# Optimization experiments

Hardware: AMD Instinct MI355X
Metric: run time of the kernel (lower is better)

## Reference

```python
import jax, jax.numpy as jnp
import numpy as np

N_NODES, N_EDGES, D_FEAT, D_HID, K_CHEB = 30000, 480000, 256, 256, 2


def setup_inputs() -> dict:
    N, E, D, H, K = N_NODES, N_EDGES, D_FEAT, D_HID, K_CHEB
    key = jax.random.key(0)
    ks = jax.random.split(key, 24)
    sD = 1.0 / np.sqrt(D)
    sH = 1.0 / np.sqrt(H)
    inp = {
        "x": jax.random.normal(ks[0], (N, D), jnp.float32),
        "edge_index": jax.random.randint(ks[1], (2, E), 0, N),
        "edge_weight": jax.random.uniform(ks[2], (E,), jnp.float32),
        "h": jax.random.normal(ks[3], (N, H), jnp.float32),
        "c": jax.random.normal(ks[4], (N, H), jnp.float32),
        "src_neighbor_ids": jax.random.randint(ks[5], (E,), 0, N),
        "dst_neighbor_ids": jax.random.randint(ks[6], (E,), 0, N),
    }
    for j, nm in enumerate(["W_i", "W_f", "W_g", "W_o"]):
        inp[nm] = jax.random.normal(ks[7 + j], (D, H), jnp.float32) * sD
    for j, nm in enumerate(["Wc_i", "Wc_f", "Wc_g", "Wc_o"]):
        inp[nm] = jax.random.normal(ks[11 + j], (K, H, H), jnp.float32) * sH
    for nm in ["bc_i", "bc_f", "bc_g", "bc_o", "b_i", "b_f", "b_g", "b_o", "b_lin"]:
        inp[nm] = jnp.zeros((H,), jnp.float32)
    for j, nm in enumerate(["w_ci", "w_cf", "w_co"]):
        inp[nm] = jax.random.normal(ks[15 + j], (H,), jnp.float32) * 0.1
    inp["W_lin"] = jax.random.normal(ks[18], (H, H), jnp.float32) * sH
    return inp


def _cheb_conv(h, src, dst, norm, W, b):
    # ChebConv, K=2, sym norm, lambda_max=2: T0 = h, T1 = L_hat h = -D^-1/2 A D^-1/2 h
    out = h @ W[0]
    t1 = jax.ops.segment_sum(norm[:, None] * h[src], dst, num_segments=h.shape[0])
    return out + t1 @ W[1] + b


def reference(x, edge_index, edge_weight, h, c, src_neighbor_ids, dst_neighbor_ids,
              W_i, W_f, W_g, W_o, Wc_i, Wc_f, Wc_g, Wc_o,
              bc_i, bc_f, bc_g, bc_o, w_ci, w_cf, w_co,
              b_i, b_f, b_g, b_o, W_lin, b_lin):
    src, dst = edge_index[0], edge_index[1]
    n = x.shape[0]
    # neighbor-feature augmentation: gather both BEFORE any update, then scatter-add
    snf = x[src_neighbor_ids]
    dnf = x[dst_neighbor_ids]
    x = x.at[src].add(snf)
    x = x.at[dst].add(dnf)
    # symmetric Chebyshev normalization (lambda_max = 2 -> diagonal of L_hat is 0)
    deg = jax.ops.segment_sum(edge_weight, src, num_segments=n)
    dinv = jnp.where(deg > 0, jax.lax.rsqrt(jnp.maximum(deg, 1e-12)), 0.0)
    norm = -dinv[src] * edge_weight * dinv[dst]
    # GCLSTM gates
    i = jax.nn.sigmoid(x @ W_i + _cheb_conv(h, src, dst, norm, Wc_i, bc_i) + w_ci * c + b_i)
    f = jax.nn.sigmoid(x @ W_f + _cheb_conv(h, src, dst, norm, Wc_f, bc_f) + w_cf * c + b_f)
    g = jnp.tanh(x @ W_g + _cheb_conv(h, src, dst, norm, Wc_g, bc_g) + b_g)
    c_new = f * c + i * g
    o = jax.nn.sigmoid(x @ W_o + _cheb_conv(h, src, dst, norm, Wc_o, bc_o) + w_co * c_new + b_o)
    h0 = o * jnp.tanh(c_new)
    h_out = jax.nn.relu(h0) @ W_lin + b_lin
    return (h_out, h0, c_new)
```

## Files before the change

kernel.cpp:

```cpp
#include <hip/hip_runtime.h>
#include <math.h>

#define NN 30000
#define NE 480000
#define DH 256
#define NH (NN * DH)
#define MPAD 30080
#define CAP 64

typedef _Float16 f16x2 __attribute__((ext_vector_type(2)));
typedef _Float16 f16x4 __attribute__((ext_vector_type(4)));
typedef _Float16 f16x8 __attribute__((ext_vector_type(8)));
typedef float f32x4 __attribute__((ext_vector_type(4)));

static __device__ __forceinline__ float sigmoidf_(float x) {
    return 1.0f / (1.0f + __expf(-x));
}
static __device__ __forceinline__ float tanhf_(float x) {
    return 1.0f - 2.0f / (1.0f + __expf(2.0f * x));
}

static __device__ __forceinline__ void gload16(const _Float16* g, _Float16* l) {
    __builtin_amdgcn_global_load_lds(
        (const __attribute__((address_space(1))) void*)g,
        (__attribute__((address_space(3))) void*)l, 16, 0, 0);
}


__global__ void deg_kernel(const int* __restrict__ src, const float* __restrict__ ew,
                           float* __restrict__ deg) {
    int e = blockIdx.x * blockDim.x + threadIdx.x;
    if (e < NE) atomicAdd(&deg[src[e]], ew[e]);
}


__global__ void mega1(const int* __restrict__ src, const int* __restrict__ dst,
                      const int* __restrict__ snf, const int* __restrict__ dnf,
                      const float* __restrict__ ew, const float* __restrict__ deg,
                      int* __restrict__ cntS, int* __restrict__ cntD,
                      int* __restrict__ slotS, int2* __restrict__ slotD,
                      const float* __restrict__ x, _Float16* __restrict__ x16,
                      const float* __restrict__ h, _Float16* __restrict__ h16,
                      const float* __restrict__ W_i, const float* __restrict__ W_f,
                      const float* __restrict__ W_g, const float* __restrict__ W_o,
                      const float* __restrict__ Wc_i, const float* __restrict__ Wc_f,
                      const float* __restrict__ Wc_g, const float* __restrict__ Wc_o,
                      const float* __restrict__ W_lin,
                      const float* __restrict__ bc_i, const float* __restrict__ bc_f,
                      const float* __restrict__ bc_g, const float* __restrict__ bc_o,
                      const float* __restrict__ b_i, const float* __restrict__ b_f,
                      const float* __restrict__ b_g, const float* __restrict__ b_o,
                      const float* __restrict__ w_ci, const float* __restrict__ w_cf,
                      const float* __restrict__ w_co,
                      _Float16* __restrict__ WcatT, _Float16* __restrict__ WlinT,
                      float4* __restrict__ bias4, float4* __restrict__ wc4) {
    int b = blockIdx.x;
    if (b < 1875) {
        int e = b * 256 + threadIdx.x;
        int s = src[e], d = dst[e];
        int pS = atomicAdd(&cntS[s], 1);
        if (pS < CAP) slotS[s * CAP + pS] = snf[e];
        float ds_ = deg[s], dd_ = deg[d];
        float is_ = (ds_ > 0.0f) ? rsqrtf(fmaxf(ds_, 1e-12f)) : 0.0f;
        float id_ = (dd_ > 0.0f) ? rsqrtf(fmaxf(dd_, 1e-12f)) : 0.0f;
        float nrm = -is_ * ew[e] * id_;
        int pD = atomicAdd(&cntD[d], 1);
        if (pD < CAP) slotD[d * CAP + pD] = make_int2(s | (dnf[e] << 15), __float_as_int(nrm));
        return;
    }
    b -= 1875;
    if (b < 7500) {
        int i = b * 256 + threadIdx.x;
        const int n8 = NN * 32;
        const float* in; _Float16* out; int idx;
        if (i < n8) { in = x; out = x16; idx = i; }
        else { in = h; out = h16; idx = i - n8; }
        const float4 p = *reinterpret_cast<const float4*>(&in[(size_t)idx * 8]);
        const float4 q = *reinterpret_cast<const float4*>(&in[(size_t)idx * 8 + 4]);
        f16x8 v;
        v[0] = (_Float16)p.x; v[1] = (_Float16)p.y; v[2] = (_Float16)p.z; v[3] = (_Float16)p.w;
        v[4] = (_Float16)q.x; v[5] = (_Float16)q.y; v[6] = (_Float16)q.z; v[7] = (_Float16)q.w;
        *reinterpret_cast<f16x8*>(&out[(size_t)idx * 8]) = v;
        return;
    }
    b -= 7500;
    int idx = b * 256 + threadIdx.x;
    if (idx < 768 * 1024) {
        int k = idx >> 10, n = idx & 1023;
        int seg = k >> 8, kk = k & 255, nn = n >> 2, gate = n & 3;
        const float* p;
        if (seg == 0) {
            p = (gate == 0) ? W_i : (gate == 1) ? W_f : (gate == 2) ? W_g : W_o;
        } else {
            const float* base = (gate == 0) ? Wc_i : (gate == 1) ? Wc_f : (gate == 2) ? Wc_g : Wc_o;
            p = base + (seg - 1) * 65536;
        }
        WcatT[(size_t)n * 768 + k] = (_Float16)p[kk * 256 + nn];
    } else if (idx < 768 * 1024 + 256 * 256) {
        int i2 = idx - 768 * 1024;
        int k = i2 >> 8, n = i2 & 255;
        WlinT[(size_t)n * 256 + k] = (_Float16)W_lin[k * 256 + n];
    } else {
        int f = idx - (768 * 1024 + 256 * 256);
        bias4[f] = make_float4(bc_i[f] + b_i[f], bc_f[f] + b_f[f],
                               bc_g[f] + b_g[f], bc_o[f] + b_o[f]);
        wc4[f] = make_float4(w_ci[f], w_cf[f], w_co[f], 0.f);
    }
}


__global__ __launch_bounds__(256) void fused_gather(const _Float16* __restrict__ x16,
                                                    const _Float16* __restrict__ h16,
                                                    const int* __restrict__ cntS,
                                                    const int* __restrict__ cntD,
                                                    const int4* __restrict__ slotS4,
                                                    const int4* __restrict__ slotD4,
                                                    _Float16* __restrict__ A16) {
    int wid = (blockIdx.x * blockDim.x + threadIdx.x) >> 6;
    int l = threadIdx.x & 63;
    if (wid >= MPAD) return;
    size_t rb = (size_t)wid * 768;
    if (wid >= NN) {
        f16x4 z = {};
        *reinterpret_cast<f16x4*>(&A16[rb + l * 4]) = z;
        *reinterpret_cast<f16x4*>(&A16[rb + 256 + l * 4]) = z;
        *reinterpret_cast<f16x4*>(&A16[rb + 512 + l * 4]) = z;
        return;
    }
    int nS = min(cntS[wid], CAP);
    int nD = min(cntD[wid], CAP);

    f16x4 xv = *reinterpret_cast<const f16x4*>(&x16[(size_t)wid * 256 + l * 4]);
    f16x4 hrow = *reinterpret_cast<const f16x4*>(&h16[(size_t)wid * 256 + l * 4]);
    float a0 = (float)xv[0], a1 = (float)xv[1], a2 = (float)xv[2], a3 = (float)xv[3];
    float t0 = 0.f, t1 = 0.f, t2 = 0.f, t3 = 0.f;

    const int4* pS = &slotS4[(size_t)wid * (CAP / 4)];
    for (int j = 0; j < nS; j += 4) {
        int4 e = pS[j >> 2];
        f16x4 v0, v1, v2, v3;
        v0 = *reinterpret_cast<const f16x4*>(&x16[(size_t)e.x * 256 + l * 4]);
        if (j + 1 < nS) v1 = *reinterpret_cast<const f16x4*>(&x16[(size_t)e.y * 256 + l * 4]);
        if (j + 2 < nS) v2 = *reinterpret_cast<const f16x4*>(&x16[(size_t)e.z * 256 + l * 4]);
        if (j + 3 < nS) v3 = *reinterpret_cast<const f16x4*>(&x16[(size_t)e.w * 256 + l * 4]);
        a0 += (float)v0[0]; a1 += (float)v0[1]; a2 += (float)v0[2]; a3 += (float)v0[3];
        if (j + 1 < nS) { a0 += (float)v1[0]; a1 += (float)v1[1]; a2 += (float)v1[2]; a3 += (float)v1[3]; }
        if (j + 2 < nS) { a0 += (float)v2[0]; a1 += (float)v2[1]; a2 += (float)v2[2]; a3 += (float)v2[3]; }
        if (j + 3 < nS) { a0 += (float)v3[0]; a1 += (float)v3[1]; a2 += (float)v3[2]; a3 += (float)v3[3]; }
    }

    const int4* pD = &slotD4[(size_t)wid * (CAP / 2)];
    for (int j = 0; j < nD; j += 4) {
        int4 ea = pD[(j >> 2) * 2];
        int4 eb = pD[(j >> 2) * 2 + 1];
        int p0 = ea.x, p1 = ea.z, p2 = eb.x, p3 = eb.z;
        float n0 = __int_as_float(ea.y), n1f = __int_as_float(ea.w);
        float n2f = __int_as_float(eb.y), n3f = __int_as_float(eb.w);
        f16x4 x0, x1, x2, x3, g0, g1, g2, g3;
        x0 = *reinterpret_cast<const f16x4*>(&x16[(size_t)(p0 >> 15) * 256 + l * 4]);
        g0 = *reinterpret_cast<const f16x4*>(&h16[(size_t)(p0 & 0x7fff) * 256 + l * 4]);
        if (j + 1 < nD) {
            x1 = *reinterpret_cast<const f16x4*>(&x16[(size_t)(p1 >> 15) * 256 + l * 4]);
            g1 = *reinterpret_cast<const f16x4*>(&h16[(size_t)(p1 & 0x7fff) * 256 + l * 4]);
        }
        if (j + 2 < nD) {
            x2 = *reinterpret_cast<const f16x4*>(&x16[(size_t)(p2 >> 15) * 256 + l * 4]);
            g2 = *reinterpret_cast<const f16x4*>(&h16[(size_t)(p2 & 0x7fff) * 256 + l * 4]);
        }
        if (j + 3 < nD) {
            x3 = *reinterpret_cast<const f16x4*>(&x16[(size_t)(p3 >> 15) * 256 + l * 4]);
            g3 = *reinterpret_cast<const f16x4*>(&h16[(size_t)(p3 & 0x7fff) * 256 + l * 4]);
        }
        a0 += (float)x0[0]; a1 += (float)x0[1]; a2 += (float)x0[2]; a3 += (float)x0[3];
        t0 += n0 * (float)g0[0]; t1 += n0 * (float)g0[1];
        t2 += n0 * (float)g0[2]; t3 += n0 * (float)g0[3];
        if (j + 1 < nD) {
            a0 += (float)x1[0]; a1 += (float)x1[1]; a2 += (float)x1[2]; a3 += (float)x1[3];
            t0 += n1f * (float)g1[0]; t1 += n1f * (float)g1[1];
            t2 += n1f * (float)g1[2]; t3 += n1f * (float)g1[3];
        }
        if (j + 2 < nD) {
            a0 += (float)x2[0]; a1 += (float)x2[1]; a2 += (float)x2[2]; a3 += (float)x2[3];
            t0 += n2f * (float)g2[0]; t1 += n2f * (float)g2[1];
            t2 += n2f * (float)g2[2]; t3 += n2f * (float)g2[3];
        }
        if (j + 3 < nD) {
            a0 += (float)x3[0]; a1 += (float)x3[1]; a2 += (float)x3[2]; a3 += (float)x3[3];
            t0 += n3f * (float)g3[0]; t1 += n3f * (float)g3[1];
            t2 += n3f * (float)g3[2]; t3 += n3f * (float)g3[3];
        }
    }

    f16x4 oX, oT;
    oX[0] = (_Float16)a0; oX[1] = (_Float16)a1; oX[2] = (_Float16)a2; oX[3] = (_Float16)a3;
    oT[0] = (_Float16)t0; oT[1] = (_Float16)t1; oT[2] = (_Float16)t2; oT[3] = (_Float16)t3;
    *reinterpret_cast<f16x4*>(&A16[rb + l * 4]) = oX;
    *reinterpret_cast<f16x4*>(&A16[rb + 256 + l * 4]) = hrow;
    *reinterpret_cast<f16x4*>(&A16[rb + 512 + l * 4]) = oT;
}


template <int K, int N, bool HALF_OUT>
__global__ __launch_bounds__(256) void gemm16(const _Float16* __restrict__ A,
                                              const _Float16* __restrict__ B,
                                              const float* __restrict__ bias,
                                              _Float16* __restrict__ outH,
                                              float* __restrict__ outF) {
    __shared__ _Float16 As[128 * 64];
    __shared__ _Float16 Bs[128 * 64];
    int tid = threadIdx.x;
    int w = tid >> 6, l = tid & 63;
    int wy = w >> 1, wx = w & 1;
    constexpr int NT = N / 128;
    constexpr int TOT = (MPAD / 128) * NT;
    constexpr int Q = TOT / 8, R = TOT & 7;
    int b = blockIdx.x;
    int xcd = b & 7, i = b >> 3;
    int v = (xcd < R ? xcd * (Q + 1) : R * (Q + 1) + (xcd - R) * Q) + i;
    int bm = (v / NT) * 128, bn = (v % NT) * 128;

    f32x4 acc[4][4];
    #pragma unroll
    for (int m = 0; m < 4; ++m)
        #pragma unroll
        for (int n = 0; n < 4; ++n)
            acc[m][n] = (f32x4){0.f, 0.f, 0.f, 0.f};

    int rowi = tid >> 3;
    int g = (tid & 7) ^ (rowi & 7);
    const _Float16* gA0 = A + (size_t)(bm + rowi) * K + g * 8;
    const _Float16* gB0 = B + (size_t)(bn + rowi) * K + g * 8;

    for (int kt = 0; kt < K; kt += 64) {
        #pragma unroll
        for (int i2 = 0; i2 < 4; ++i2) {
            gload16(gA0 + kt + (size_t)i2 * 32 * K, &As[i2 * 2048 + w * 512]);
            gload16(gB0 + kt + (size_t)i2 * 32 * K, &Bs[i2 * 2048 + w * 512]);
        }
        __syncthreads();

        f16x8 af[4][2], bf[4][2];
        #pragma unroll
        for (int m = 0; m < 4; ++m) {
            int row = wy * 64 + m * 16 + (l & 15);
            #pragma unroll
            for (int ks = 0; ks < 2; ++ks) {
                int ch = (ks * 4 + (l >> 4)) ^ (l & 7);
                af[m][ks] = *reinterpret_cast<const f16x8*>(&As[row * 64 + ch * 8]);
            }
        }
        #pragma unroll
        for (int n = 0; n < 4; ++n) {
            int row = wx * 64 + n * 16 + (l & 15);
            #pragma unroll
            for (int ks = 0; ks < 2; ++ks) {
                int ch = (ks * 4 + (l >> 4)) ^ (l & 7);
                bf[n][ks] = *reinterpret_cast<const f16x8*>(&Bs[row * 64 + ch * 8]);
            }
        }
        #pragma unroll
        for (int ks = 0; ks < 2; ++ks)
            #pragma unroll
            for (int m = 0; m < 4; ++m)
                #pragma unroll
                for (int n = 0; n < 4; ++n)
                    acc[m][n] = __builtin_amdgcn_mfma_f32_16x16x32_f16(
                        af[m][ks], bf[n][ks], acc[m][n], 0, 0, 0);
        __syncthreads();
    }

    #pragma unroll
    for (int m = 0; m < 4; ++m) {
        #pragma unroll
        for (int n = 0; n < 4; ++n) {
            int col = bn + wx * 64 + n * 16 + (l & 15);
            #pragma unroll
            for (int j = 0; j < 4; ++j) {
                int row = bm + wy * 64 + m * 16 + (l >> 4) * 4 + j;
                if (row < NN) {
                    if constexpr (HALF_OUT)
                        outH[(size_t)row * N + col] = (_Float16)acc[m][n][j];
                    else
                        outF[(size_t)row * N + col] = acc[m][n][j] + bias[col];
                }
            }
        }
    }
}


__global__ void gate_kernel(const _Float16* __restrict__ pre, const float* __restrict__ c,
                            const float4* __restrict__ bias4, const float4* __restrict__ wc4,
                            float* __restrict__ h0p, float* __restrict__ cnp,
                            _Float16* __restrict__ relu16) {
    int idx = blockIdx.x * blockDim.x + threadIdx.x;
    if (idx >= MPAD * 128) return;
    int row = idx >> 7, f0 = (idx & 127) << 1;
    size_t o = (size_t)row * 256 + f0;
    if (row >= NN) {
        *reinterpret_cast<f16x2*>(&relu16[o]) = (f16x2){(_Float16)0.f, (_Float16)0.f};
        return;
    }
    f16x8 pv = *reinterpret_cast<const f16x8*>(&pre[(size_t)row * 1024 + f0 * 4]);
    float2 cv = *reinterpret_cast<const float2*>(&c[o]);
    float4 b4a = bias4[f0], b4b = bias4[f0 + 1];
    float4 w4a = wc4[f0], w4b = wc4[f0 + 1];
    float iv0 = sigmoidf_((float)pv[0] + b4a.x + w4a.x * cv.x);
    float fv0 = sigmoidf_((float)pv[1] + b4a.y + w4a.y * cv.x);
    float gv0 = tanhf_((float)pv[2] + b4a.z);
    float cn0 = fv0 * cv.x + iv0 * gv0;
    float ov0 = sigmoidf_((float)pv[3] + b4a.w + w4a.z * cn0);
    float h00 = ov0 * tanhf_(cn0);
    float iv1 = sigmoidf_((float)pv[4] + b4b.x + w4b.x * cv.y);
    float fv1 = sigmoidf_((float)pv[5] + b4b.y + w4b.y * cv.y);
    float gv1 = tanhf_((float)pv[6] + b4b.z);
    float cn1 = fv1 * cv.y + iv1 * gv1;
    float ov1 = sigmoidf_((float)pv[7] + b4b.w + w4b.z * cn1);
    float h01 = ov1 * tanhf_(cn1);
    *reinterpret_cast<float2*>(&cnp[o]) = make_float2(cn0, cn1);
    *reinterpret_cast<float2*>(&h0p[o]) = make_float2(h00, h01);
    *reinterpret_cast<f16x2*>(&relu16[o]) =
        (f16x2){(_Float16)fmaxf(h00, 0.f), (_Float16)fmaxf(h01, 0.f)};
}


extern "C" void kernel_launch(void* const* d_in, const int* in_sizes, int n_in,
                              void* d_out, int out_size, void* d_ws, size_t ws_size,
                              hipStream_t stream) {
    const float* x   = (const float*)d_in[0];
    const int*   ei  = (const int*)d_in[1];
    const float* ew  = (const float*)d_in[2];
    const float* h   = (const float*)d_in[3];
    const float* c   = (const float*)d_in[4];
    const int*   snf = (const int*)d_in[5];
    const int*   dnf = (const int*)d_in[6];
    const float* W_i = (const float*)d_in[7];
    const float* W_f = (const float*)d_in[8];
    const float* W_g = (const float*)d_in[9];
    const float* W_o = (const float*)d_in[10];
    const float* Wc_i = (const float*)d_in[11];
    const float* Wc_f = (const float*)d_in[12];
    const float* Wc_g = (const float*)d_in[13];
    const float* Wc_o = (const float*)d_in[14];
    const float* bc_i = (const float*)d_in[15];
    const float* bc_f = (const float*)d_in[16];
    const float* bc_g = (const float*)d_in[17];
    const float* bc_o = (const float*)d_in[18];
    const float* b_i  = (const float*)d_in[19];
    const float* b_f  = (const float*)d_in[20];
    const float* b_g  = (const float*)d_in[21];
    const float* b_o  = (const float*)d_in[22];
    const float* b_lin = (const float*)d_in[23];
    const float* w_ci = (const float*)d_in[24];
    const float* w_cf = (const float*)d_in[25];
    const float* w_co = (const float*)d_in[26];
    const float* W_lin = (const float*)d_in[27];

    const int* src = ei;
    const int* dst = ei + NE;

    float* out = (float*)d_out;
    float* houtp = out;
    float* h0p   = out + NH;
    float* cnp   = out + 2 * NH;

    char* ws = (char*)d_ws;
    _Float16* pre16 = (_Float16*)ws;
    int* cntS = (int*)ws;
    int* cntD = (int*)(ws + 131072);
    float* deg = (float*)(ws + 262144);
    int* slotS = (int*)(ws + 393216);
    int2* slotD = (int2*)(ws + 8073216);
    _Float16* h16 = (_Float16*)(ws + 23433216);

    _Float16* A16 = (_Float16*)(ws + 61440000);
    _Float16* relu16 = A16;
    _Float16* WcatT = (_Float16*)(ws + 107642880);
    _Float16* WlinT = (_Float16*)(ws + 109215744);
    float4* bias4 = (float4*)(ws + 109346816);
    float4* wc4 = (float4*)(ws + 109350912);
    _Float16* x16 = (_Float16*)(ws + 109477888);

    hipMemsetAsync(ws, 0, 393216, stream);

    deg_kernel<<<1875, 256, 0, stream>>>(src, ew, deg);

    mega1<<<12704, 256, 0, stream>>>(src, dst, snf, dnf, ew, deg,
                                     cntS, cntD, slotS, slotD,
                                     x, x16, h, h16,
                                     W_i, W_f, W_g, W_o, Wc_i, Wc_f, Wc_g, Wc_o, W_lin,
                                     bc_i, bc_f, bc_g, bc_o, b_i, b_f, b_g, b_o,
                                     w_ci, w_cf, w_co,
                                     WcatT, WlinT, bias4, wc4);

    fused_gather<<<7520, 256, 0, stream>>>(x16, h16, cntS, cntD,
                                           (const int4*)slotS, (const int4*)slotD, A16);

    gemm16<768, 1024, true><<<1880, 256, 0, stream>>>(A16, WcatT, nullptr, pre16, nullptr);

    gate_kernel<<<15040, 256, 0, stream>>>(pre16, c, bias4, wc4, h0p, cnp, relu16);

    gemm16<256, 256, false><<<470, 256, 0, stream>>>(relu16, WlinT, b_lin, nullptr, houtp);
}
```

Before: 318.7 us.

## Fold degree pass into mega1, defer norm to gather, double-buffer big GEMM

The separate degree kernel is folded into mega1 as extra blocks. Edge normalization is no longer computed at slot-fill time; the raw edge weight is stored and the norm is computed inside fused_gather from deg. The main 768x1024 GEMM gets a double-buffered LDS pipeline using explicit vmcnt waits and barriers to overlap global loads with MFMA. Risk: deg atomics in the same grid as the slot fill that previously read deg now race, though norm is moved later, so this is consistent. Extra deg gathers per edge in fused_gather, and doubled LDS lowers occupancy.

```diff
diff --git a/kernel.cpp b/kernel.cpp
--- a/kernel.cpp
+++ b/kernel.cpp
@@ -19,6 +19,9 @@
 static __device__ __forceinline__ float tanhf_(float x) {
     return 1.0f - 2.0f / (1.0f + __expf(2.0f * x));
 }
+static __device__ __forceinline__ float rsq_(float d) {
+    return (d > 0.0f) ? rsqrtf(fmaxf(d, 1e-12f)) : 0.0f;
+}
 
 static __device__ __forceinline__ void gload16(const _Float16* g, _Float16* l) {
     __builtin_amdgcn_global_load_lds(
@@ -27,16 +30,9 @@
 }
 
 
-__global__ void deg_kernel(const int* __restrict__ src, const float* __restrict__ ew,
-                           float* __restrict__ deg) {
-    int e = blockIdx.x * blockDim.x + threadIdx.x;
-    if (e < NE) atomicAdd(&deg[src[e]], ew[e]);
-}
-
-
 __global__ void mega1(const int* __restrict__ src, const int* __restrict__ dst,
                       const int* __restrict__ snf, const int* __restrict__ dnf,
-                      const float* __restrict__ ew, const float* __restrict__ deg,
+                      const float* __restrict__ ew, float* __restrict__ deg,
                       int* __restrict__ cntS, int* __restrict__ cntD,
                       int* __restrict__ slotS, int2* __restrict__ slotD,
                       const float* __restrict__ x, _Float16* __restrict__ x16,
@@ -57,15 +53,18 @@
     int b = blockIdx.x;
     if (b < 1875) {
         int e = b * 256 + threadIdx.x;
+        atomicAdd(&deg[src[e]], ew[e]);
+        return;
+    }
+    b -= 1875;
+    if (b < 1875) {
+        int e = b * 256 + threadIdx.x;
         int s = src[e], d = dst[e];
         int pS = atomicAdd(&cntS[s], 1);
         if (pS < CAP) slotS[s * CAP + pS] = snf[e];
-        float ds_ = deg[s], dd_ = deg[d];
-        float is_ = (ds_ > 0.0f) ? rsqrtf(fmaxf(ds_, 1e-12f)) : 0.0f;
-        float id_ = (dd_ > 0.0f) ? rsqrtf(fmaxf(dd_, 1e-12f)) : 0.0f;
-        float nrm = -is_ * ew[e] * id_;
         int pD = atomicAdd(&cntD[d], 1);
-        if (pD < CAP) slotD[d * CAP + pD] = make_int2(s | (dnf[e] << 15), __float_as_int(nrm));
+        if (pD < CAP) slotD[d * CAP + pD] = make_int2(s | (dnf[e] << 15),
+                                                      __float_as_int(ew[e]));
         return;
     }
     b -= 1875;
@@ -115,6 +114,7 @@
                                                     const int* __restrict__ cntD,
                                                     const int4* __restrict__ slotS4,
                                                     const int4* __restrict__ slotD4,
+                                                    const float* __restrict__ deg,
                                                     _Float16* __restrict__ A16) {
     int wid = (blockIdx.x * blockDim.x + threadIdx.x) >> 6;
     int l = threadIdx.x & 63;
@@ -129,6 +129,7 @@
     }
     int nS = min(cntS[wid], CAP);
     int nD = min(cntD[wid], CAP);
+    float dv = rsq_(deg[wid]);
 
     f16x4 xv = *reinterpret_cast<const f16x4*>(&x16[(size_t)wid * 256 + l * 4]);
     f16x4 hrow = *reinterpret_cast<const f16x4*>(&h16[(size_t)wid * 256 + l * 4]);
@@ -154,40 +155,50 @@
         int4 ea = pD[(j >> 2) * 2];
         int4 eb = pD[(j >> 2) * 2 + 1];
         int p0 = ea.x, p1 = ea.z, p2 = eb.x, p3 = eb.z;
-        float n0 = __int_as_float(ea.y), n1f = __int_as_float(ea.w);
-        float n2f = __int_as_float(eb.y), n3f = __int_as_float(eb.w);
+        int s0 = p0 & 0x7fff, s1 = p1 & 0x7fff, s2 = p2 & 0x7fff, s3 = p3 & 0x7fff;
+        float w0 = __int_as_float(ea.y), w1 = __int_as_float(ea.w);
+        float w2 = __int_as_float(eb.y), w3 = __int_as_float(eb.w);
         f16x4 x0, x1, x2, x3, g0, g1, g2, g3;
+        float dg0 = 0.f, dg1 = 0.f, dg2 = 0.f, dg3 = 0.f;
         x0 = *reinterpret_cast<const f16x4*>(&x16[(size_t)(p0 >> 15) * 256 + l * 4]);
-        g0 = *reinterpret_cast<const f16x4*>(&h16[(size_t)(p0 & 0x7fff) * 256 + l * 4]);
+        g0 = *reinterpret_cast<const f16x4*>(&h16[(size_t)s0 * 256 + l * 4]);
+        dg0 = deg[s0];
         if (j + 1 < nD) {
             x1 = *reinterpret_cast<const f16x4*>(&x16[(size_t)(p1 >> 15) * 256 + l * 4]);
-            g1 = *reinterpret_cast<const f16x4*>(&h16[(size_t)(p1 & 0x7fff) * 256 + l * 4]);
+            g1 = *reinterpret_cast<const f16x4*>(&h16[(size_t)s1 * 256 + l * 4]);
+            dg1 = deg[s1];
         }
         if (j + 2 < nD) {
             x2 = *reinterpret_cast<const f16x4*>(&x16[(size_t)(p2 >> 15) * 256 + l * 4]);
-            g2 = *reinterpret_cast<const f16x4*>(&h16[(size_t)(p2 & 0x7fff) * 256 + l * 4]);
+            g2 = *reinterpret_cast<const f16x4*>(&h16[(size_t)s2 * 256 + l * 4]);
+            dg2 = deg[s2];
         }
         if (j + 3 < nD) {
             x3 = *reinterpret_cast<const f16x4*>(&x16[(size_t)(p3 >> 15) * 256 + l * 4]);
-            g3 = *reinterpret_cast<const f16x4*>(&h16[(size_t)(p3 & 0x7fff) * 256 + l * 4]);
-        }
+            g3 = *reinterpret_cast<const f16x4*>(&h16[(size_t)s3 * 256 + l * 4]);
+            dg3 = deg[s3];
+        }
+        float n0 = -rsq_(dg0) * w0 * dv;
+        float n1 = -rsq_(dg1) * w1 * dv;
+        float n2 = -rsq_(dg2) * w2 * dv;
+        float n3 = -rsq_(dg3) * w3 * dv;
         a0 += (float)x0[0]; a1 += (float)x0[1]; a2 += (float)x0[2]; a3 += (float)x0[3];
         t0 += n0 * (float)g0[0]; t1 += n0 * (float)g0[1];
         t2 += n0 * (float)g0[2]; t3 += n0 * (float)g0[3];
         if (j + 1 < nD) {
             a0 += (float)x1[0]; a1 += (float)x1[1]; a2 += (float)x1[2]; a3 += (float)x1[3];
-            t0 += n1f * (float)g1[0]; t1 += n1f * (float)g1[1];
-            t2 += n1f * (float)g1[2]; t3 += n1f * (float)g1[3];
+            t0 += n1 * (float)g1[0]; t1 += n1 * (float)g1[1];
+            t2 += n1 * (float)g1[2]; t3 += n1 * (float)g1[3];
         }
         if (j + 2 < nD) {
             a0 += (float)x2[0]; a1 += (float)x2[1]; a2 += (float)x2[2]; a3 += (float)x2[3];
-            t0 += n2f * (float)g2[0]; t1 += n2f * (float)g2[1];
-            t2 += n2f * (float)g2[2]; t3 += n2f * (float)g2[3];
+            t0 += n2 * (float)g2[0]; t1 += n2 * (float)g2[1];
+            t2 += n2 * (float)g2[2]; t3 += n2 * (float)g2[3];
         }
         if (j + 3 < nD) {
             a0 += (float)x3[0]; a1 += (float)x3[1]; a2 += (float)x3[2]; a3 += (float)x3[3];
-            t0 += n3f * (float)g3[0]; t1 += n3f * (float)g3[1];
-            t2 += n3f * (float)g3[2]; t3 += n3f * (float)g3[3];
+            t0 += n3 * (float)g3[0]; t1 += n3 * (float)g3[1];
+            t2 += n3 * (float)g3[2]; t3 += n3 * (float)g3[3];
         }
     }
 
@@ -200,14 +211,52 @@
 }
 
 
-template <int K, int N, bool HALF_OUT>
+#define STAGE(AS, BS, KT)                                                          \
+    {                                                                              \
+        _Pragma("unroll")                                                          \
+        for (int i2_ = 0; i2_ < 4; ++i2_) {                                        \
+            gload16(gA0 + (KT) + (size_t)i2_ * 32 * K, &AS[i2_ * 2048 + w * 512]); \
+            gload16(gB0 + (KT) + (size_t)i2_ * 32 * K, &BS[i2_ * 2048 + w * 512]); \
+        }                                                                          \
+    }
+
+#define COMPUTE(AS, BS)                                                            \
+    {                                                                              \
+        f16x8 af_[4][2], bf_[4][2];                                                \
+        _Pragma("unroll")                                                          \
+        for (int m_ = 0; m_ < 4; ++m_) {                                           \
+            int row_ = wy * 64 + m_ * 16 + (l & 15);                               \
+            _Pragma("unroll")                                                      \
+            for (int ks_ = 0; ks_ < 2; ++ks_) {                                    \
+                int ch_ = (ks_ * 4 + (l >> 4)) ^ (l & 7);                          \
+                af_[m_][ks_] = *reinterpret_cast<const f16x8*>(&AS[row_ * 64 + ch_ * 8]); \
+            }                                                                      \
+        }                                                                          \
+        _Pragma("unroll")                                                          \
+        for (int n_ = 0; n_ < 4; ++n_) {                                           \
+            int row_ = wx * 64 + n_ * 16 + (l & 15);                               \
+            _Pragma("unroll")                                                      \
+            for (int ks_ = 0; ks_ < 2; ++ks_) {                                    \
+                int ch_ = (ks_ * 4 + (l >> 4)) ^ (l & 7);                          \
+                bf_[n_][ks_] = *reinterpret_cast<const f16x8*>(&BS[row_ * 64 + ch_ * 8]); \
+            }                                                                      \
+        }                                                                          \
+        _Pragma("unroll")                                                          \
+        for (int ks_ = 0; ks_ < 2; ++ks_)                                          \
+            _Pragma("unroll")                                                      \
+            for (int m_ = 0; m_ < 4; ++m_)                                         \
+                _Pragma("unroll")                                                  \
+                for (int n_ = 0; n_ < 4; ++n_)                                     \
+                    acc[m_][n_] = __builtin_amdgcn_mfma_f32_16x16x32_f16(          \
+                        af_[m_][ks_], bf_[n_][ks_], acc[m_][n_], 0, 0, 0);         \
+    }
+
+template <int K, int N, bool HALF_OUT, bool DBUF>
 __global__ __launch_bounds__(256) void gemm16(const _Float16* __restrict__ A,
                                               const _Float16* __restrict__ B,
                                               const float* __restrict__ bias,
                                               _Float16* __restrict__ outH,
                                               float* __restrict__ outF) {
-    __shared__ _Float16 As[128 * 64];
-    __shared__ _Float16 Bs[128 * 64];
     int tid = threadIdx.x;
     int w = tid >> 6, l = tid & 63;
     int wy = w >> 1, wx = w & 1;
@@ -231,42 +280,43 @@
     const _Float16* gA0 = A + (size_t)(bm + rowi) * K + g * 8;
     const _Float16* gB0 = B + (size_t)(bn + rowi) * K + g * 8;
 
-    for (int kt = 0; kt < K; kt += 64) {
+    if constexpr (DBUF) {
+        static_assert(K % 128 == 0, "DBUF path needs an even K-step count");
+        __shared__ _Float16 As0[8192];
+        __shared__ _Float16 Bs0[8192];
+        __shared__ _Float16 As1[8192];
+        __shared__ _Float16 Bs1[8192];
+        STAGE(As0, Bs0, 0);
         #pragma unroll
-        for (int i2 = 0; i2 < 4; ++i2) {
-            gload16(gA0 + kt + (size_t)i2 * 32 * K, &As[i2 * 2048 + w * 512]);
-            gload16(gB0 + kt + (size_t)i2 * 32 * K, &Bs[i2 * 2048 + w * 512]);
-        }
-        __syncthreads();
-
-        f16x8 af[4][2], bf[4][2];
-        #pragma unroll
-        for (int m = 0; m < 4; ++m) {
-            int row = wy * 64 + m * 16 + (l & 15);
-            #pragma unroll
-            for (int ks = 0; ks < 2; ++ks) {
-                int ch = (ks * 4 + (l >> 4)) ^ (l & 7);
-                af[m][ks] = *reinterpret_cast<const f16x8*>(&As[row * 64 + ch * 8]);
+        for (int kt0 = 0; kt0 < K; kt0 += 128) {
+            if (kt0 + 64 < K) {
+                STAGE(As1, Bs1, kt0 + 64);
+                asm volatile("s_waitcnt vmcnt(8)" ::: "memory");
+            } else {
+                asm volatile("s_waitcnt vmcnt(0)" ::: "memory");
             }
-        }
-        #pragma unroll
-        for (int n = 0; n < 4; ++n) {
-            int row = wx * 64 + n * 16 + (l & 15);
-            #pragma unroll
-            for (int ks = 0; ks < 2; ++ks) {
-                int ch = (ks * 4 + (l >> 4)) ^ (l & 7);
-                bf[n][ks] = *reinterpret_cast<const f16x8*>(&Bs[row * 64 + ch * 8]);
+            asm volatile("s_barrier" ::: "memory");
+            COMPUTE(As0, Bs0);
+            asm volatile("s_barrier" ::: "memory");
+            if (kt0 + 128 < K) {
+                STAGE(As0, Bs0, kt0 + 128);
+                asm volatile("s_waitcnt vmcnt(8)" ::: "memory");
+            } else {
+                asm volatile("s_waitcnt vmcnt(0)" ::: "memory");
             }
-        }
-        #pragma unroll
-        for (int ks = 0; ks < 2; ++ks)
-            #pragma unroll
-            for (int m = 0; m < 4; ++m)
-                #pragma unroll
-                for (int n = 0; n < 4; ++n)
-                    acc[m][n] = __builtin_amdgcn_mfma_f32_16x16x32_f16(
-                        af[m][ks], bf[n][ks], acc[m][n], 0, 0, 0);
-        __syncthreads();
+            asm volatile("s_barrier" ::: "memory");
+            COMPUTE(As1, Bs1);
+            asm volatile("s_barrier" ::: "memory");
+        }
+    } else {
+        __shared__ _Float16 As[8192];
+        __shared__ _Float16 Bs[8192];
+        for (int kt = 0; kt < K; kt += 64) {
+            STAGE(As, Bs, kt);
+            __syncthreads();
+            COMPUTE(As, Bs);
+            __syncthreads();
+        }
     }
 
     #pragma unroll
@@ -383,9 +433,7 @@
 
     hipMemsetAsync(ws, 0, 393216, stream);
 
-    deg_kernel<<<1875, 256, 0, stream>>>(src, ew, deg);
-
-    mega1<<<12704, 256, 0, stream>>>(src, dst, snf, dnf, ew, deg,
+    mega1<<<14579, 256, 0, stream>>>(src, dst, snf, dnf, ew, deg,
                                      cntS, cntD, slotS, slotD,
                                      x, x16, h, h16,
                                      W_i, W_f, W_g, W_o, Wc_i, Wc_f, Wc_g, Wc_o, W_lin,
@@ -394,11 +442,12 @@
                                      WcatT, WlinT, bias4, wc4);
 
     fused_gather<<<7520, 256, 0, stream>>>(x16, h16, cntS, cntD,
-                                           (const int4*)slotS, (const int4*)slotD, A16);
-
-    gemm16<768, 1024, true><<<1880, 256, 0, stream>>>(A16, WcatT, nullptr, pre16, nullptr);
+                                           (const int4*)slotS, (const int4*)slotD,
+                                           deg, A16);
+
+    gemm16<768, 1024, true, true><<<1880, 256, 0, stream>>>(A16, WcatT, nullptr, pre16, nullptr);
 
     gate_kernel<<<15040, 256, 0, stream>>>(pre16, c, bias4, wc4, h0p, cnp, relu16);
 
-    gemm16<256, 256, false><<<470, 256, 0, stream>>>(relu16, WlinT, b_lin, nullptr, houtp);
-}
+    gemm16<256, 256, false, false><<<470, 256, 0, stream>>>(relu16, WlinT, b_lin, nullptr, houtp);
+}
```

Result: no change. 316.0 us (-0.8%).
